# Optimization experiments

Measured on AMD Instinct MI355X. Metric: run time of the kernel, lower is better.

The kernel has to match this reference:

```python
import jax, jax.numpy as jnp
import numpy as np

B, S, E, D, H, L, V = 8, 128, 512, 1024, 16, 4, 32000
DH = D // H
FF = 4 * D
SCALE = 1.0 / (DH ** 0.5)
NEG = -1e30


def _layer_norm(x, g, b, eps=1e-5):
    m = jnp.mean(x, axis=-1, keepdims=True)
    v = jnp.mean((x - m) ** 2, axis=-1, keepdims=True)
    return (x - m) / jnp.sqrt(v + eps) * g + b


def _rel_shift(x):
    # x: [q, k, b, n] -> TransformerXL relative shift
    q, k, b, n = x.shape
    xp = jnp.concatenate([jnp.zeros((q, 1, b, n), x.dtype), x], axis=1)
    xp = xp.reshape(k + 1, q, b, n)
    return xp[1:].reshape(q, k, b, n)


def setup_inputs():
    key = jax.random.key(0)
    ks = jax.random.split(key, 40)
    g = lambda i, shape, s=0.02: jax.random.normal(ks[i], shape, jnp.float32) * s
    inp = {
        'input_ids': jax.random.randint(ks[0], (B, E), 0, V),
        'encoder_rep': jax.random.normal(ks[1], (B, E, D), jnp.float32),
        'input_mask': jnp.ones((B, E), jnp.float32),
        'decode_input': jax.random.randint(ks[2], (B, S), 0, V),
        'decode_target': jax.random.randint(ks[3], (B, S), 0, V),
        'word_emb': g(4, (V, D)),
        'qkv_w': g(5, (L, 3 * D, D)), 'r_w': g(6, (L, D, D)), 'o_w': g(7, (L, D, D)),
        'kv_w': g(8, (L, 2 * D, D)), 'q_w': g(9, (L, D, D)), 'io_w': g(10, (L, D, D)),
        'rr_bias': g(11, (L, H, DH)), 'rw_bias': g(12, (L, H, DH)),
        'ln1_g': jnp.ones((L, D)), 'ln1_b': jnp.zeros((L, D)),
        'ln2_g': jnp.ones((L, D)), 'ln2_b': jnp.zeros((L, D)),
        'ffn_w1': g(13, (L, FF, D)), 'ffn_b1': jnp.zeros((L, FF)),
        'ffn_w2': g(14, (L, D, FF)), 'ffn_b2': jnp.zeros((L, D)),
        'ln3_g': jnp.ones((L, D)), 'ln3_b': jnp.zeros((L, D)),
        'out_w': g(15, (D, D)), 'out_b': jnp.zeros((D,)),
        'copy_w': g(16, (D, D)), 'copy_b': jnp.zeros((D,)),
        'mode_w': g(17, (1, D)), 'mode_b': jnp.zeros((1,)),
    }
    return inp


def _forward(input_ids, encoder_rep, input_mask, decode_input, decode_target,
             word_emb, qkv_w, r_w, o_w, kv_w, q_w, io_w, rr_bias, rw_bias,
             ln1_g, ln1_b, ln2_g, ln2_b, ffn_w1, ffn_b1, ffn_w2, ffn_b2,
             ln3_g, ln3_b, out_w, out_b, copy_w, copy_b, mode_w, mode_b):
    # relative position embedding r: [S, D]
    pos_seq = jnp.arange(S - 1, -1, -1.0, dtype=jnp.float32)
    inv_freq = 1.0 / (10000.0 ** (jnp.arange(0.0, D, 2.0) / D))
    sin_inp = pos_seq[:, None] * inv_freq[None, :]
    r = jnp.concatenate([jnp.sin(sin_inp), jnp.cos(sin_inp)], axis=-1)

    causal = jnp.tril(jnp.ones((S, S), jnp.bool_))[:, :, None, None]  # [i,j,1,1]
    enc_mask_t = input_mask.T  # [E, B]

    core = word_emb[decode_input].transpose(1, 0, 2)  # [S, B, D]
    enc_t = encoder_rep.transpose(1, 0, 2)            # [E, B, D]

    for l in range(L):
        w = core
        heads = w @ qkv_w[l].T  # [S,B,3D]
        q, k, v = jnp.split(heads, 3, axis=-1)
        q = q.reshape(S, B, H, DH); k = k.reshape(S, B, H, DH); v = v.reshape(S, B, H, DH)
        r_k = (r @ r_w[l].T).reshape(S, H, DH)
        AC = jnp.einsum('ibnd,jbnd->ijbn', q + rw_bias[l], k)
        BD = _rel_shift(jnp.einsum('ibnd,jnd->ijbn', q + rr_bias[l], r_k))
        score = (AC + BD) * SCALE
        score = jnp.where(causal, score, NEG)
        prob = jax.nn.softmax(score, axis=1)
        vec = jnp.einsum('ijbn,jbnd->ibnd', prob, v).reshape(S, B, D)
        x = _layer_norm(w + vec @ o_w[l].T, ln1_g[l], ln1_b[l])

        # cross attention
        kv = enc_t @ kv_w[l].T
        k2, v2 = jnp.split(kv, 2, axis=-1)
        k2 = k2.reshape(E, B, H, DH); v2 = v2.reshape(E, B, H, DH)
        q2 = (x @ q_w[l].T).reshape(S, B, H, DH)
        score2 = jnp.einsum('qbnd,kbnd->qkbn', q2, k2) * SCALE
        score2 = score2 + (1.0 - enc_mask_t)[None, :, :, None] * NEG
        prob2 = jax.nn.softmax(score2, axis=1)
        vec2 = jnp.einsum('ijbn,jbnd->ibnd', prob2, v2).reshape(S, B, D)
        y = _layer_norm(x + vec2 @ io_w[l].T, ln2_g[l], ln2_b[l])

        # FFN (exact GELU as torch nn.GELU default)
        h = jax.nn.gelu(y @ ffn_w1[l].T + ffn_b1[l], approximate=False)
        h = h @ ffn_w2[l].T + ffn_b2[l]
        core = _layer_norm(y + h, ln3_g[l], ln3_b[l])

    core_out = core.transpose(1, 0, 2)  # [B, S, D]
    output = core_out @ out_w.T + out_b
    vocab_logits = output @ word_emb.T  # [B,S,V]
    vocab_prob = jax.nn.softmax(vocab_logits, axis=-1)

    copy_h = core_out @ copy_w.T + copy_b
    input_logits = jnp.einsum('bid,bjd->bij', copy_h, encoder_rep)
    input_logits = input_logits + (1.0 - input_mask[:, None, :]) * NEG
    input_prob = jax.nn.softmax(input_logits, axis=-1)  # [B,S,E]

    mode_sig = jax.nn.sigmoid(core_out @ mode_w.T + mode_b)  # [B,S,1]
    vocab_prob = vocab_prob * mode_sig

    idx = jnp.broadcast_to(input_ids[:, None, :], (B, S, E))
    b_i = jnp.arange(B)[:, None, None]
    s_i = jnp.arange(S)[None, :, None]
    vocab_prob = vocab_prob.at[b_i, s_i, idx].add((1.0 - mode_sig) * input_prob)

    flat = vocab_prob.reshape(-1, V)
    tgt = decode_target.reshape(-1)
    predict = jnp.take_along_axis(flat, tgt[:, None], axis=1)[:, 0]
    valid = (tgt != 0).astype(jnp.float32)
    loss = jnp.sum(-jnp.log(predict + 1e-6) * valid) / jnp.sum(valid)
    return jnp.repeat(loss[None], B)


def reference(input_ids, encoder_rep, input_mask, decode_input, decode_target,
              word_emb, qkv_w, r_w, o_w, kv_w, q_w, io_w, rr_bias, rw_bias,
              ln1_g, ln1_b, ln2_g, ln2_b, ffn_w1, ffn_b1, ffn_w2, ffn_b2,
              ln3_g, ln3_b, out_w, out_b, copy_w, copy_b, mode_w, mode_b):
    return _forward(input_ids, encoder_rep, input_mask, decode_input, decode_target,
                    word_emb, qkv_w, r_w, o_w, kv_w, q_w, io_w, rr_bias, rw_bias,
                    ln1_g, ln1_b, ln2_g, ln2_b, ffn_w1, ffn_b1, ffn_w2, ffn_b2,
                    ln3_g, ln3_b, out_w, out_b, copy_w, copy_b, mode_w, mode_b)
```

## Files before the change

kernel.cpp:

```cpp
#include <hip/hip_runtime.h>
#include <math.h>

#define B_ 8
#define S_ 128
#define E_ 512
#define D_ 1024
#define H_ 16
#define L_ 4
#define V_ 32000
#define DH_ 64
#define FF_ 4096
#define M_ 1024
#define ME_ 4096
#define NT_ 125
#define SCALE_F 0.125f
#define NEGV (-1e30f)

typedef __attribute__((ext_vector_type(8))) short short8;
typedef __attribute__((ext_vector_type(4))) float f32x4;

__device__ __forceinline__ float bf2f(ushort u) {
  union { unsigned int u32; float f; } v; v.u32 = ((unsigned int)u) << 16; return v.f;
}
__device__ __forceinline__ ushort f2bf(float x) {
  union { float f; unsigned int u; } v; v.f = x;
  unsigned int r = v.u + 0x7fff + ((v.u >> 16) & 1);
  return (ushort)(r >> 16);
}
__device__ __forceinline__ void gl_lds16(const ushort* g, ushort* l) {
  __builtin_amdgcn_global_load_lds((const __attribute__((address_space(1))) void*)g,
                                   (__attribute__((address_space(3))) void*)l, 16, 0, 0);
}

__device__ __forceinline__ float warp_reduce_sum(float v) {
#pragma unroll
  for (int o = 32; o > 0; o >>= 1) v += __shfl_down(v, o);
  return v;
}
__device__ __forceinline__ float warp_reduce_max(float v) {
#pragma unroll
  for (int o = 32; o > 0; o >>= 1) v = fmaxf(v, __shfl_down(v, o));
  return v;
}
__device__ __forceinline__ float block_reduce_sum(float v, float* sred) {
  v = warp_reduce_sum(v);
  __syncthreads();
  if ((threadIdx.x & 63) == 0) sred[threadIdx.x >> 6] = v;
  __syncthreads();
  float s = 0.0f;
  int nw = blockDim.x >> 6;
  for (int w = 0; w < nw; ++w) s += sred[w];
  return s;
}
__device__ __forceinline__ float block_reduce_max(float v, float* sred) {
  v = warp_reduce_max(v);
  __syncthreads();
  if ((threadIdx.x & 63) == 0) sred[threadIdx.x >> 6] = v;
  __syncthreads();
  float s = -3.4e38f;
  int nw = blockDim.x >> 6;
  for (int w = 0; w < nw; ++w) s = fmaxf(s, sred[w]);
  return s;
}

__global__ __launch_bounds__(256) void castf_kernel(const float* __restrict__ in,
                                                    ushort* __restrict__ out, int n4) {
  int t = blockIdx.x * 256 + threadIdx.x;
  if (t >= n4) return;
  float4 v = ((const float4*)in)[t];
  ushort4 o;
  o.x = f2bf(v.x); o.y = f2bf(v.y); o.z = f2bf(v.z); o.w = f2bf(v.w);
  ((ushort4*)out)[t] = o;
}

__global__ __launch_bounds__(256) void castlayer_kernel(
    const float* __restrict__ sqkv, const float* __restrict__ so,
    const float* __restrict__ sq, const float* __restrict__ sio,
    const float* __restrict__ sf1, const float* __restrict__ sf2,
    ushort* __restrict__ dqkv, ushort* __restrict__ dov,
    ushort* __restrict__ dq, ushort* __restrict__ dio,
    ushort* __restrict__ df1, ushort* __restrict__ df2) {
  int t = blockIdx.x * 256 + threadIdx.x;
  const float* src; ushort* dst; int idx;
  if (t < 786432)       { src = sqkv; dst = dqkv; idx = t; }
  else if (t < 1048576) { src = so;  dst = dov; idx = t - 786432; }
  else if (t < 1310720) { src = sq;  dst = dq;  idx = t - 1048576; }
  else if (t < 1572864) { src = sio; dst = dio; idx = t - 1310720; }
  else if (t < 2621440) { src = sf1; dst = df1; idx = t - 1572864; }
  else if (t < 3670016) { src = sf2; dst = df2; idx = t - 2621440; }
  else return;
  float4 v = ((const float4*)src)[idx];
  ushort4 o4;
  o4.x = f2bf(v.x); o4.y = f2bf(v.y); o4.z = f2bf(v.z); o4.w = f2bf(v.w);
  ((ushort4*)dst)[idx] = o4;
}

__global__ __launch_bounds__(256) void enct_kernel(const float* __restrict__ enc,
                                                   ushort* __restrict__ encT) {
  int t = blockIdx.x * 256 + threadIdx.x;
  if (t >= ME_ * D_) return;
  int d = t & (D_ - 1);
  int row = t >> 10;
  int e = row >> 3, b = row & 7;
  encT[t] = f2bf(enc[((size_t)b * E_ + e) * D_ + d]);
}

__global__ __launch_bounds__(256) void pos_emb_kernel(ushort* __restrict__ r) {
  int t = blockIdx.x * 256 + threadIdx.x;
  if (t >= S_ * D_) return;
  int i = t / D_, j = t % D_;
  float pos = (float)(S_ - 1 - i);
  int jj = (j < D_ / 2) ? j : (j - D_ / 2);
  float invf = powf(10000.0f, -(float)(2 * jj) / (float)D_);
  float a = pos * invf;
  r[t] = f2bf((j < D_ / 2) ? sinf(a) : cosf(a));
}

__global__ __launch_bounds__(256) void embed_kernel(const int* __restrict__ ids,
                                                    const float* __restrict__ emb,
                                                    float* __restrict__ core,
                                                    ushort* __restrict__ core_bf) {
  int t = blockIdx.x * 256 + threadIdx.x;
  if (t >= M_ * D_) return;
  int d = t & (D_ - 1);
  int row = t >> 10;
  int s = row >> 3, b = row & 7;
  float v = emb[(size_t)ids[b * S_ + s] * D_ + d];
  core[t] = v;
  core_bf[t] = f2bf(v);
}

template <int EPI>
__global__ __launch_bounds__(256) void gemm_w_kernel(
    const ushort* __restrict__ A, const ushort* __restrict__ Bm,
    const float* __restrict__ bias, void* __restrict__ Cv,
    int M, int N, int K, int ksplit,
    long long Arow, long long Abatch, long long Brow, long long Bbatch,
    long long Crow, long long Cbatch, long long Csplit) {
  __shared__ ushort lA[128 * 32];
  __shared__ ushort lB[128 * 32];
  int tid = threadIdx.x;
  int bz = blockIdx.z;
  int batch = bz / ksplit, split = bz % ksplit;
  int kLen = K / ksplit, kStart = split * kLen;
  const ushort* Ab = A + (size_t)batch * Abatch;
  const ushort* Bb = Bm + (size_t)batch * Bbatch;
  int bm = blockIdx.y * 128, bn = blockIdx.x * 128;
  int lane = tid & 63, wave = tid >> 6;
  int wrow = (wave >> 1) * 64, wcol = (wave & 1) * 64;
  int quad = lane >> 4, l16 = lane & 15;
  f32x4 acc[4][4];
#pragma unroll
  for (int i = 0; i < 4; ++i)
#pragma unroll
    for (int j = 0; j < 4; ++j) { acc[i][j][0] = 0.f; acc[i][j][1] = 0.f; acc[i][j][2] = 0.f; acc[i][j][3] = 0.f; }
  int r0 = tid >> 2, c0 = (tid & 3) * 8;
  int r1 = (tid + 256) >> 2;
  for (int k0 = kStart; k0 < kStart + kLen; k0 += 32) {
    __syncthreads();
    gl_lds16(Ab + (size_t)(bm + r0) * Arow + k0 + c0, &lA[(size_t)tid * 8]);
    gl_lds16(Ab + (size_t)(bm + r1) * Arow + k0 + c0, &lA[(size_t)(256 + tid) * 8]);
    gl_lds16(Bb + (size_t)(bn + r0) * Brow + k0 + c0, &lB[(size_t)tid * 8]);
    gl_lds16(Bb + (size_t)(bn + r1) * Brow + k0 + c0, &lB[(size_t)(256 + tid) * 8]);
    __syncthreads();
    short8 af[4], bfr[4];
#pragma unroll
    for (int mi = 0; mi < 4; ++mi)
      af[mi] = *(const short8*)&lA[(size_t)(wrow + mi * 16 + l16) * 32 + quad * 8];
#pragma unroll
    for (int ni = 0; ni < 4; ++ni)
      bfr[ni] = *(const short8*)&lB[(size_t)(wcol + ni * 16 + l16) * 32 + quad * 8];
#pragma unroll
    for (int mi = 0; mi < 4; ++mi)
#pragma unroll
      for (int ni = 0; ni < 4; ++ni)
        acc[mi][ni] = __builtin_amdgcn_mfma_f32_16x16x32_bf16(af[mi], bfr[ni], acc[mi][ni], 0, 0, 0);
  }
#pragma unroll
  for (int mi = 0; mi < 4; ++mi) {
    int row0 = bm + wrow + mi * 16 + quad * 4;
#pragma unroll
    for (int ni = 0; ni < 4; ++ni) {
      int col = bn + wcol + ni * 16 + l16;
      float bv = 0.f;
      if (EPI >= 3) bv = bias[col];
#pragma unroll
      for (int r = 0; r < 4; ++r) {
        float v = acc[mi][ni][r] + bv;
        if (EPI == 4) v = 0.5f * v * (1.0f + erff(v * 0.70710678118654752f));
        size_t ci = (size_t)split * Csplit + (size_t)batch * Cbatch + (size_t)(row0 + r) * Crow + col;
        if (EPI == 0) ((float*)Cv)[ci] = v;
        else ((ushort*)Cv)[ci] = f2bf(v);
      }
    }
  }
}

template <int EPI>
__global__ __launch_bounds__(512, 2) void gemm256_kernel(
    const ushort* __restrict__ A, const ushort* __restrict__ Bm, void* __restrict__ Cv,
    float* __restrict__ tmax, float* __restrict__ tsum,
    long long Arow, long long Abatch, long long Brow, long long Bbatch,
    long long Crow, long long Cbatch) {
  __shared__ ushort sT[4][2][2][128 * 32];
  __shared__ float smax[256][4];
  __shared__ float ssum[256][4];
  const int NK = 32;
  int tid = threadIdx.x;
  int bm, bn, bnT = 0, batch = 0;
  if constexpr (EPI == 5) {
    int orig = blockIdx.x;
    int xcd = orig & 7;
    int base = (xcd < 4) ? xcd * 63 : 4 * 63 + (xcd - 4) * 62;
    int wg = base + (orig >> 3);
    bm = (wg & 3) * 256;
    bnT = wg >> 2;
    bn = bnT * 256;
  } else {
    bn = blockIdx.x * 256;
    bm = blockIdx.y * 256;
    batch = blockIdx.z;
  }
  const ushort* Ab = A + (size_t)batch * Abatch;
  const ushort* Bb = Bm + (size_t)batch * Bbatch;
  int lane = tid & 63, wave = tid >> 6;
  int wr = wave >> 2;
  int wc = wave & 3;
  int bhalf = wc >> 1;
  int brow0 = (wc & 1) * 64;
  int quad = lane >> 4, l16 = lane & 15;
  int sr = tid >> 2, sc = (tid & 3) * 8;

  f32x4 acc[8][4];
#pragma unroll
  for (int i = 0; i < 8; ++i)
#pragma unroll
    for (int j = 0; j < 4; ++j) { acc[i][j][0]=0.f; acc[i][j][1]=0.f; acc[i][j][2]=0.f; acc[i][j][3]=0.f; }

#define STAGE_HALF(s_, ab_, h_)                                                        \
  do {                                                                                 \
    int s__ = (s_); int b__ = s__ & 3;                                                 \
    if ((ab_) == 0)                                                                    \
      gl_lds16(Ab + (size_t)(bm + (h_) * 128 + sr) * Arow + s__ * 32 + sc,             \
               &sT[b__][0][h_][tid * 8]);                                              \
    else                                                                               \
      gl_lds16(Bb + (size_t)(bn + (h_) * 128 + sr) * Brow + s__ * 32 + sc,             \
               &sT[b__][1][h_][tid * 8]);                                              \
  } while (0)

#pragma unroll
  for (int s = 0; s < 3; ++s) {
    STAGE_HALF(s, 0, 0); STAGE_HALF(s, 0, 1);
    STAGE_HALF(s, 1, 0); STAGE_HALF(s, 1, 1);
  }
  asm volatile("s_waitcnt vmcnt(8)");
  __builtin_amdgcn_s_barrier();
  __builtin_amdgcn_sched_barrier(0);

  short8 af[4], bfv[4];
  for (int t = 0; t < NK; ++t) {
    int bt = t & 3;
#pragma unroll
    for (int i = 0; i < 4; ++i)
      af[i] = *(const short8*)&sT[bt][0][wr][(i * 16 + l16) * 32 + quad * 8];
#pragma unroll
    for (int i = 0; i < 4; ++i)
      bfv[i] = *(const short8*)&sT[bt][1][bhalf][(brow0 + i * 16 + l16) * 32 + quad * 8];
    if (t + 3 < NK) { STAGE_HALF(t + 3, 0, 0); STAGE_HALF(t + 3, 0, 1); }
    __builtin_amdgcn_s_barrier();
    __builtin_amdgcn_sched_barrier(0);
    __builtin_amdgcn_s_setprio(1);
#pragma unroll
    for (int mi = 0; mi < 4; ++mi)
#pragma unroll
      for (int ni = 0; ni < 4; ++ni)
        acc[mi][ni] = __builtin_amdgcn_mfma_f32_16x16x32_bf16(af[mi], bfv[ni], acc[mi][ni], 0, 0, 0);
    __builtin_amdgcn_s_setprio(0);
    __builtin_amdgcn_s_barrier();
    __builtin_amdgcn_sched_barrier(0);
#pragma unroll
    for (int i = 0; i < 4; ++i)
      af[i] = *(const short8*)&sT[bt][0][wr][((4 + i) * 16 + l16) * 32 + quad * 8];
    if (t + 3 < NK) { STAGE_HALF(t + 3, 1, 0); STAGE_HALF(t + 3, 1, 1); }
    if (t + 3 < NK)      asm volatile("s_waitcnt vmcnt(8)");
    else if (t + 2 < NK) asm volatile("s_waitcnt vmcnt(4)");
    else                 asm volatile("s_waitcnt vmcnt(0)");
    __builtin_amdgcn_s_barrier();
    __builtin_amdgcn_sched_barrier(0);
    __builtin_amdgcn_s_setprio(1);
#pragma unroll
    for (int mi = 0; mi < 4; ++mi)
#pragma unroll
      for (int ni = 0; ni < 4; ++ni)
        acc[4 + mi][ni] = __builtin_amdgcn_mfma_f32_16x16x32_bf16(af[mi], bfv[ni], acc[4 + mi][ni], 0, 0, 0);
    __builtin_amdgcn_s_setprio(0);
    __builtin_amdgcn_s_barrier();
    __builtin_amdgcn_sched_barrier(0);
  }
#undef STAGE_HALF

  if constexpr (EPI == 5) {
#pragma unroll
    for (int mi = 0; mi < 8; ++mi)
#pragma unroll
      for (int r = 0; r < 4; ++r) {
        int rr = wr * 128 + mi * 16 + quad * 4 + r;
        float lm = -3.4e38f;
#pragma unroll
        for (int ni = 0; ni < 4; ++ni) lm = fmaxf(lm, acc[mi][ni][r]);
#pragma unroll
        for (int o = 1; o < 16; o <<= 1) lm = fmaxf(lm, __shfl_xor(lm, o));
        if (l16 == 0) smax[rr][wc] = lm;
      }
    __syncthreads();
#pragma unroll
    for (int mi = 0; mi < 8; ++mi)
#pragma unroll
      for (int r = 0; r < 4; ++r) {
        int rr = wr * 128 + mi * 16 + quad * 4 + r;
        float m = fmaxf(fmaxf(smax[rr][0], smax[rr][1]), fmaxf(smax[rr][2], smax[rr][3]));
        float ls = 0.f;
#pragma unroll
        for (int ni = 0; ni < 4; ++ni) ls += __expf(acc[mi][ni][r] - m);
#pragma unroll
        for (int o = 1; o < 16; o <<= 1) ls += __shfl_xor(ls, o);
        if (l16 == 0) ssum[rr][wc] = ls;
      }
    __syncthreads();
    if (tid < 256) {
      float m = fmaxf(fmaxf(smax[tid][0], smax[tid][1]), fmaxf(smax[tid][2], smax[tid][3]));
      float s = ssum[tid][0] + ssum[tid][1] + ssum[tid][2] + ssum[tid][3];
      tmax[(size_t)(bm + tid) * NT_ + bnT] = m;
      tsum[(size_t)(bm + tid) * NT_ + bnT] = s;
    }
  } else {
    ushort* C = (ushort*)Cv + (size_t)batch * Cbatch;
#pragma unroll
    for (int mi = 0; mi < 8; ++mi) {
      int row0 = bm + wr * 128 + mi * 16 + quad * 4;
#pragma unroll
      for (int ni = 0; ni < 4; ++ni) {
        int col = bn + wc * 64 + ni * 16 + l16;
#pragma unroll
        for (int r = 0; r < 4; ++r)
          C[(size_t)(row0 + r) * Crow + col] = f2bf(acc[mi][ni][r]);
      }
    }
  }
}

__global__ __launch_bounds__(256) void vocab_combine_kernel(const float* __restrict__ tmax,
                                                            const float* __restrict__ tsum,
                                                            float* __restrict__ rmax,
                                                            float* __restrict__ rsum) {
  __shared__ float sred[4];
  int m = blockIdx.x;
  float mx = -3.4e38f;
  for (int t = threadIdx.x; t < NT_; t += 256) mx = fmaxf(mx, tmax[(size_t)m * NT_ + t]);
  mx = block_reduce_max(mx, sred);
  float s = 0.f;
  for (int t = threadIdx.x; t < NT_; t += 256)
    s += tsum[(size_t)m * NT_ + t] * expf(tmax[(size_t)m * NT_ + t] - mx);
  s = block_reduce_sum(s, sred);
  if (threadIdx.x == 0) { rmax[m] = mx; rsum[m] = s; }
}

__global__ __launch_bounds__(256) void tlogit_kernel(const ushort* __restrict__ headout,
                                                     const ushort* __restrict__ emb,
                                                     const int* __restrict__ tgt,
                                                     float* __restrict__ tl) {
  __shared__ float sred[4];
  int m = blockIdx.x;
  int s = m >> 3, b = m & 7;
  int t = tgt[b * S_ + s];
  const ushort* a = headout + (size_t)m * 2048;
  const ushort* w = emb + (size_t)t * D_;
  float acc = 0.f;
  for (int i = threadIdx.x; i < D_; i += 256) acc += bf2f(a[i]) * bf2f(w[i]);
  acc = block_reduce_sum(acc, sred);
  if (threadIdx.x == 0) tl[m] = acc;
}

__global__ __launch_bounds__(256) void attn1_fused_kernel(const ushort* __restrict__ heads,
                                                          const ushort* __restrict__ rkproj,
                                                          const float* __restrict__ rw,
                                                          const float* __restrict__ rr,
                                                          ushort* __restrict__ attnA) {
  __shared__ float score[128][129];
  __shared__ ushort pP[128][136];
  __shared__ ushort vT[64][136];
  int bz = blockIdx.x;
  int b = bz >> 4, n = bz & 15;
  int tid = threadIdx.x, lane = tid & 63, wave = tid >> 6;
  int quad = lane >> 4, l16 = lane & 15;
  int wrow = wave * 32;

  {
    int j = tid >> 1, dbase = (tid & 1) * 32;
    const ushort* src = heads + (size_t)(j * 8 + b) * 3072 + 2048 + n * 64 + dbase;
#pragma unroll
    for (int c8 = 0; c8 < 4; ++c8) {
      short8 v8 = *(const short8*)(src + c8 * 8);
#pragma unroll
      for (int cc = 0; cc < 8; ++cc) vT[dbase + c8 * 8 + cc][j] = (ushort)v8[cc];
    }
  }

  short8 qrw[2][2], qrr[2][2];
#pragma unroll
  for (int mi = 0; mi < 2; ++mi) {
    int i = wrow + mi * 16 + l16;
    const ushort* qp = heads + (size_t)(i * 8 + b) * 3072 + n * 64;
#pragma unroll
    for (int kc = 0; kc < 2; ++kc) {
      int k0 = kc * 32 + quad * 8;
      short8 qv = *(const short8*)(qp + k0);
      short8 w, rv;
#pragma unroll
      for (int t = 0; t < 8; ++t) {
        float q = bf2f((ushort)qv[t]);
        w[t] = (short)f2bf(q + rw[n * 64 + k0 + t]);
        rv[t] = (short)f2bf(q + rr[n * 64 + k0 + t]);
      }
      qrw[mi][kc] = w; qrr[mi][kc] = rv;
    }
  }

  {
    f32x4 acc[2][8];
#pragma unroll
    for (int i = 0; i < 2; ++i)
#pragma unroll
      for (int j = 0; j < 8; ++j) { acc[i][j][0]=0.f; acc[i][j][1]=0.f; acc[i][j][2]=0.f; acc[i][j][3]=0.f; }
#pragma unroll
    for (int kc = 0; kc < 2; ++kc) {
      int k0 = kc * 32 + quad * 8;
      short8 kf[8];
#pragma unroll
      for (int ni = 0; ni < 8; ++ni) {
        int j = ni * 16 + l16;
        kf[ni] = *(const short8*)(heads + (size_t)(j * 8 + b) * 3072 + 1024 + n * 64 + k0);
      }
#pragma unroll
      for (int mi = 0; mi < 2; ++mi)
#pragma unroll
        for (int ni = 0; ni < 8; ++ni)
          acc[mi][ni] = __builtin_amdgcn_mfma_f32_16x16x32_bf16(qrw[mi][kc], kf[ni], acc[mi][ni], 0, 0, 0);
    }
#pragma unroll
    for (int mi = 0; mi < 2; ++mi)
#pragma unroll
      for (int ni = 0; ni < 8; ++ni)
#pragma unroll
        for (int r = 0; r < 4; ++r)
          score[wrow + mi * 16 + quad * 4 + r][ni * 16 + l16] = acc[mi][ni][r];
  }
  {
    f32x4 acc[2][8];
#pragma unroll
    for (int i = 0; i < 2; ++i)
#pragma unroll
      for (int j = 0; j < 8; ++j) { acc[i][j][0]=0.f; acc[i][j][1]=0.f; acc[i][j][2]=0.f; acc[i][j][3]=0.f; }
#pragma unroll
    for (int kc = 0; kc < 2; ++kc) {
      int k0 = kc * 32 + quad * 8;
      short8 rkf[8];
#pragma unroll
      for (int ni = 0; ni < 8; ++ni) {
        int jp = ni * 16 + l16;
        rkf[ni] = *(const short8*)(rkproj + (size_t)jp * 1024 + n * 64 + k0);
      }
#pragma unroll
      for (int mi = 0; mi < 2; ++mi)
#pragma unroll
        for (int ni = 0; ni < 8; ++ni)
          acc[mi][ni] = __builtin_amdgcn_mfma_f32_16x16x32_bf16(qrr[mi][kc], rkf[ni], acc[mi][ni], 0, 0, 0);
    }
#pragma unroll
    for (int mi = 0; mi < 2; ++mi)
#pragma unroll
      for (int r = 0; r < 4; ++r) {
        int i = wrow + mi * 16 + quad * 4 + r;
#pragma unroll
        for (int ni = 0; ni < 8; ++ni) {
          int jp = ni * 16 + l16;
          if (jp >= 127 - i) score[i][jp - 127 + i] += acc[mi][ni][r];
        }
      }
  }
  {
    int row = tid >> 1, halfc = (tid & 1) * 64;
    float mx = -3.4e38f;
    for (int c = halfc; c < halfc + 64; ++c) {
      float v = (c <= row) ? score[row][c] * SCALE_F : -3.4e38f;
      mx = fmaxf(mx, v);
    }
    mx = fmaxf(mx, __shfl_xor(mx, 1));
    float s = 0.f;
    for (int c = halfc; c < halfc + 64; ++c) {
      float e = (c <= row) ? __expf(score[row][c] * SCALE_F - mx) : 0.f;
      score[row][c] = e;
      s += e;
    }
    s += __shfl_xor(s, 1);
    float inv = 1.0f / s;
    for (int c = halfc; c < halfc + 64; ++c) pP[row][c] = f2bf(score[row][c] * inv);
  }
  __syncthreads();
  {
    f32x4 acc[2][4];
#pragma unroll
    for (int i = 0; i < 2; ++i)
#pragma unroll
      for (int j = 0; j < 4; ++j) { acc[i][j][0]=0.f; acc[i][j][1]=0.f; acc[i][j][2]=0.f; acc[i][j][3]=0.f; }
#pragma unroll
    for (int kc = 0; kc < 4; ++kc) {
      int k0 = kc * 32 + quad * 8;
      short8 pf[2], vf[4];
#pragma unroll
      for (int mi = 0; mi < 2; ++mi)
        pf[mi] = *(const short8*)&pP[wrow + mi * 16 + l16][k0];
#pragma unroll
      for (int ni = 0; ni < 4; ++ni)
        vf[ni] = *(const short8*)&vT[ni * 16 + l16][k0];
#pragma unroll
      for (int mi = 0; mi < 2; ++mi)
#pragma unroll
        for (int ni = 0; ni < 4; ++ni)
          acc[mi][ni] = __builtin_amdgcn_mfma_f32_16x16x32_bf16(pf[mi], vf[ni], acc[mi][ni], 0, 0, 0);
    }
#pragma unroll
    for (int mi = 0; mi < 2; ++mi)
#pragma unroll
      for (int r = 0; r < 4; ++r) {
        int i = wrow + mi * 16 + quad * 4 + r;
#pragma unroll
        for (int ni = 0; ni < 4; ++ni)
          attnA[(size_t)(i * 8 + b) * 1024 + n * 64 + ni * 16 + l16] = f2bf(acc[mi][ni][r]);
      }
  }
}

__global__ __launch_bounds__(256) void attn2_fused_kernel(const float* __restrict__ q0,
                                                          const float* __restrict__ q1,
                                                          const ushort* __restrict__ kvproj,
                                                          const float* __restrict__ mask,
                                                          ushort* __restrict__ attnA) {
  __shared__ ushort vT[64][136];
  __shared__ ushort pP[128][136];
  __shared__ float mtile[128];
  int bz = blockIdx.x;
  int b = bz >> 4, n = bz & 15;
  int tid = threadIdx.x, lane = tid & 63, wave = tid >> 6;
  int quad = lane >> 4, l16 = lane & 15;
  int wrow = wave * 32;
  short8 qf[2][2];
#pragma unroll
  for (int mi = 0; mi < 2; ++mi) {
    int i = wrow + mi * 16 + l16;
    size_t base = (size_t)(i * 8 + b) * 1024 + n * 64;
#pragma unroll
    for (int kc = 0; kc < 2; ++kc) {
      int k0 = kc * 32 + quad * 8;
      short8 v;
#pragma unroll
      for (int t = 0; t < 8; ++t) v[t] = (short)f2bf(q0[base + k0 + t] + q1[base + k0 + t]);
      qf[mi][kc] = v;
    }
  }
  float m_run[2][4], l_run[2][4];
#pragma unroll
  for (int mi = 0; mi < 2; ++mi)
#pragma unroll
    for (int r = 0; r < 4; ++r) { m_run[mi][r] = -3.0e38f; l_run[mi][r] = 0.f; }
  f32x4 accO[2][4];
#pragma unroll
  for (int i = 0; i < 2; ++i)
#pragma unroll
    for (int j = 0; j < 4; ++j) { accO[i][j][0]=0.f; accO[i][j][1]=0.f; accO[i][j][2]=0.f; accO[i][j][3]=0.f; }

  for (int et = 0; et < 4; ++et) {
    __syncthreads();
    {
      int j = tid >> 1, dbase = (tid & 1) * 32;
      int e = et * 128 + j;
      const ushort* src = kvproj + (size_t)(e * 8 + b) * 2048 + 1024 + n * 64 + dbase;
#pragma unroll
      for (int c8 = 0; c8 < 4; ++c8) {
        short8 v8 = *(const short8*)(src + c8 * 8);
#pragma unroll
        for (int cc = 0; cc < 8; ++cc) vT[dbase + c8 * 8 + cc][j] = (ushort)v8[cc];
      }
      if (tid < 128) mtile[tid] = (1.0f - mask[b * E_ + et * 128 + tid]) * NEGV;
    }
    f32x4 accS[2][8];
#pragma unroll
    for (int i = 0; i < 2; ++i)
#pragma unroll
      for (int j = 0; j < 8; ++j) { accS[i][j][0]=0.f; accS[i][j][1]=0.f; accS[i][j][2]=0.f; accS[i][j][3]=0.f; }
#pragma unroll
    for (int kc = 0; kc < 2; ++kc) {
      int k0 = kc * 32 + quad * 8;
      short8 kf[8];
#pragma unroll
      for (int ni = 0; ni < 8; ++ni) {
        int e = et * 128 + ni * 16 + l16;
        kf[ni] = *(const short8*)(kvproj + (size_t)(e * 8 + b) * 2048 + n * 64 + k0);
      }
#pragma unroll
      for (int mi = 0; mi < 2; ++mi)
#pragma unroll
        for (int ni = 0; ni < 8; ++ni)
          accS[mi][ni] = __builtin_amdgcn_mfma_f32_16x16x32_bf16(qf[mi][kc], kf[ni], accS[mi][ni], 0, 0, 0);
    }
    __syncthreads();
#pragma unroll
    for (int mi = 0; mi < 2; ++mi)
#pragma unroll
      for (int r = 0; r < 4; ++r) {
        float v[8];
        float vmax = -3.4e38f;
#pragma unroll
        for (int ni = 0; ni < 8; ++ni) {
          v[ni] = accS[mi][ni][r] * SCALE_F + mtile[ni * 16 + l16];
          vmax = fmaxf(vmax, v[ni]);
        }
#pragma unroll
        for (int o = 1; o < 16; o <<= 1) vmax = fmaxf(vmax, __shfl_xor(vmax, o));
        float mnew = fmaxf(m_run[mi][r], vmax);
        float alpha = __expf(m_run[mi][r] - mnew);
        float ls = 0.f;
        int row = wrow + mi * 16 + quad * 4 + r;
#pragma unroll
        for (int ni = 0; ni < 8; ++ni) {
          float p = __expf(v[ni] - mnew);
          ls += p;
          pP[row][ni * 16 + l16] = f2bf(p);
        }
#pragma unroll
        for (int o = 1; o < 16; o <<= 1) ls += __shfl_xor(ls, o);
        l_run[mi][r] = l_run[mi][r] * alpha + ls;
        m_run[mi][r] = mnew;
#pragma unroll
        for (int ni = 0; ni < 4; ++ni) accO[mi][ni][r] *= alpha;
      }
#pragma unroll
    for (int kc = 0; kc < 4; ++kc) {
      int k0 = kc * 32 + quad * 8;
      short8 pf[2], vf[4];
#pragma unroll
      for (int mi = 0; mi < 2; ++mi)
        pf[mi] = *(const short8*)&pP[wrow + mi * 16 + l16][k0];
#pragma unroll
      for (int ni = 0; ni < 4; ++ni)
        vf[ni] = *(const short8*)&vT[ni * 16 + l16][k0];
#pragma unroll
      for (int mi = 0; mi < 2; ++mi)
#pragma unroll
        for (int ni = 0; ni < 4; ++ni)
          accO[mi][ni] = __builtin_amdgcn_mfma_f32_16x16x32_bf16(pf[mi], vf[ni], accO[mi][ni], 0, 0, 0);
    }
  }
#pragma unroll
  for (int mi = 0; mi < 2; ++mi)
#pragma unroll
    for (int r = 0; r < 4; ++r) {
      int i = wrow + mi * 16 + quad * 4 + r;
      float inv = 1.0f / l_run[mi][r];
#pragma unroll
      for (int ni = 0; ni < 4; ++ni)
        attnA[(size_t)(i * 8 + b) * 1024 + n * 64 + ni * 16 + l16] = f2bf(accO[mi][ni][r] * inv);
    }
}

__global__ __launch_bounds__(256) void addln_kernel(const float* __restrict__ a,
                                                    const float* __restrict__ c,
                                                    int nsplit, long long cstride,
                                                    const float* __restrict__ bias,
                                                    const float* __restrict__ g,
                                                    const float* __restrict__ bb,
                                                    float* __restrict__ out,
                                                    ushort* __restrict__ out_bf) {
  __shared__ float sred[4];
  int row = blockIdx.x;
  const float* pa = a + (size_t)row * D_;
  float vals[4];
  float s = 0.f;
#pragma unroll
  for (int it = 0; it < 4; ++it) {
    int idx = threadIdx.x + it * 256;
    float v = pa[idx];
    for (int sp = 0; sp < nsplit; ++sp) v += c[(size_t)sp * cstride + (size_t)row * D_ + idx];
    if (bias) v += bias[idx];
    vals[it] = v;
    s += v;
  }
  s = block_reduce_sum(s, sred);
  float mean = s * (1.0f / D_);
  float ss = 0.f;
#pragma unroll
  for (int it = 0; it < 4; ++it) {
    float dd = vals[it] - mean;
    ss += dd * dd;
  }
  ss = block_reduce_sum(ss, sred);
  float inv = rsqrtf(ss * (1.0f / D_) + 1e-5f);
#pragma unroll
  for (int it = 0; it < 4; ++it) {
    int idx = threadIdx.x + it * 256;
    float r = (vals[it] - mean) * inv * g[idx] + bb[idx];
    out[(size_t)row * D_ + idx] = r;
    out_bf[(size_t)row * D_ + idx] = f2bf(r);
  }
}

__global__ __launch_bounds__(256) void mode_kernel(const float* __restrict__ core,
                                                   const float* __restrict__ mode_w,
                                                   const float* __restrict__ mode_b,
                                                   float* __restrict__ mode_sig) {
  __shared__ float sred[4];
  int m = blockIdx.x;
  const float* a = core + (size_t)m * D_;
  float s = 0.f;
  for (int t = threadIdx.x; t < D_; t += 256) s += a[t] * mode_w[t];
  s = block_reduce_sum(s, sred);
  if (threadIdx.x == 0) mode_sig[m] = 1.0f / (1.0f + expf(-(s + mode_b[0])));
}

__global__ __launch_bounds__(256) void final_kernel(const float* __restrict__ lg,
                                                    const int* __restrict__ ids,
                                                    const float* __restrict__ mask,
                                                    const int* __restrict__ tgt,
                                                    const float* __restrict__ mode_sig,
                                                    const float* __restrict__ tlogit,
                                                    const float* __restrict__ rmax,
                                                    const float* __restrict__ rsum,
                                                    float* __restrict__ loss_acc) {
  __shared__ float sred[4];
  int s = blockIdx.x, b = blockIdx.y;
  int m = s * B_ + b;
  size_t base = (size_t)(b * S_ + s) * E_;
  const long long LGS = (long long)B_ * S_ * E_;
  int tg = tgt[b * S_ + s];
  float lv[2];
  float mx = -3.4e38f;
#pragma unroll
  for (int it = 0; it < 2; ++it) {
    int e = threadIdx.x + it * 256;
    float raw = 0.f;
#pragma unroll
    for (int sp = 0; sp < 4; ++sp) raw += lg[sp * LGS + base + e];
    raw += (1.0f - mask[b * E_ + e]) * NEGV;
    lv[it] = raw;
    mx = fmaxf(mx, raw);
  }
  mx = block_reduce_max(mx, sred);
  float ssum = 0.f, csum = 0.f;
#pragma unroll
  for (int it = 0; it < 2; ++it) {
    int e = threadIdx.x + it * 256;
    float ev = expf(lv[it] - mx);
    ssum += ev;
    if (ids[b * E_ + e] == tg) csum += ev;
  }
  ssum = block_reduce_sum(ssum, sred);
  csum = block_reduce_sum(csum, sred);
  if (threadIdx.x == 0) {
    float copy_p = csum / ssum;
    float pv = expf(tlogit[m] - rmax[m]) / rsum[m];
    float msig = mode_sig[m];
    float predict = pv * msig + (1.0f - msig) * copy_p;
    float valid = (tg != 0) ? 1.0f : 0.0f;
    atomicAdd(&loss_acc[0], -logf(predict + 1e-6f) * valid);
    atomicAdd(&loss_acc[1], valid);
  }
}

__global__ void writeout_kernel(const float* __restrict__ loss_acc, float* __restrict__ out) {
  if (threadIdx.x < B_) out[threadIdx.x] = loss_acc[0] / loss_acc[1];
}

static void gw(hipStream_t st, int epi, const ushort* A, const ushort* B, const float* bias,
               void* C, int M, int N, int K,
               long long Ar, long long Ab, long long Br, long long Bb,
               long long Cr, long long Cb, int nb, int ksplit, long long Csplit) {
  dim3 g(N / 128, M / 128, nb * ksplit);
  switch (epi) {
    case 0: gemm_w_kernel<0><<<g, 256, 0, st>>>(A, B, bias, C, M, N, K, ksplit, Ar, Ab, Br, Bb, Cr, Cb, Csplit); break;
    case 1: gemm_w_kernel<1><<<g, 256, 0, st>>>(A, B, bias, C, M, N, K, ksplit, Ar, Ab, Br, Bb, Cr, Cb, Csplit); break;
    case 3: gemm_w_kernel<3><<<g, 256, 0, st>>>(A, B, bias, C, M, N, K, ksplit, Ar, Ab, Br, Bb, Cr, Cb, Csplit); break;
    case 4: gemm_w_kernel<4><<<g, 256, 0, st>>>(A, B, bias, C, M, N, K, ksplit, Ar, Ab, Br, Bb, Cr, Cb, Csplit); break;
  }
}
static void castTo(hipStream_t st, const float* src, ushort* dst, size_t count) {
  int n4 = (int)(count / 4);
  castf_kernel<<<(n4 + 255) / 256, 256, 0, st>>>(src, dst, n4);
}

extern "C" void kernel_launch(void* const* d_in, const int* in_sizes, int n_in,
                              void* d_out, int out_size, void* d_ws, size_t ws_size,
                              hipStream_t stream) {
  const int* input_ids = (const int*)d_in[0];
  const float* encoder_rep = (const float*)d_in[1];
  const float* input_mask = (const float*)d_in[2];
  const int* decode_input = (const int*)d_in[3];
  const int* decode_target = (const int*)d_in[4];
  const float* word_emb = (const float*)d_in[5];
  const float* qkv_w = (const float*)d_in[6];
  const float* r_w = (const float*)d_in[7];
  const float* o_w = (const float*)d_in[8];
  const float* kv_w = (const float*)d_in[9];
  const float* q_w = (const float*)d_in[10];
  const float* io_w = (const float*)d_in[11];
  const float* rr_bias = (const float*)d_in[12];
  const float* rw_bias = (const float*)d_in[13];
  const float* ln1_g = (const float*)d_in[14];
  const float* ln1_b = (const float*)d_in[15];
  const float* ln2_g = (const float*)d_in[16];
  const float* ln2_b = (const float*)d_in[17];
  const float* ffn_w1 = (const float*)d_in[18];
  const float* ffn_b1 = (const float*)d_in[19];
  const float* ffn_w2 = (const float*)d_in[20];
  const float* ffn_b2 = (const float*)d_in[21];
  const float* ln3_g = (const float*)d_in[22];
  const float* ln3_b = (const float*)d_in[23];
  const float* out_w = (const float*)d_in[24];
  const float* out_b = (const float*)d_in[25];
  const float* copy_w = (const float*)d_in[26];
  const float* copy_b = (const float*)d_in[27];
  const float* mode_w = (const float*)d_in[28];
  const float* mode_b = (const float*)d_in[29];
  float* out = (float*)d_out;

  char* base = (char*)d_ws;
  size_t off = 0;
  auto alloc = [&](size_t bytes) -> void* {
    void* p = base + off;
    off = (off + bytes + 255) & ~(size_t)255;
    return p;
  };

  ushort* wl_qkv = (ushort*)alloc((size_t)3 * D_ * D_ * 2);
  ushort* wl_o = (ushort*)alloc((size_t)D_ * D_ * 2);
  ushort* wl_q = (ushort*)alloc((size_t)D_ * D_ * 2);
  ushort* wl_io = (ushort*)alloc((size_t)D_ * D_ * 2);
  ushort* wl_f1 = (ushort*)alloc((size_t)FF_ * D_ * 2);
  ushort* wl_f2 = (ushort*)alloc((size_t)FF_ * D_ * 2);
  ushort* wl_kv = (ushort*)alloc((size_t)L_ * 2 * D_ * D_ * 2);
  ushort* wl_r = (ushort*)alloc((size_t)L_ * D_ * D_ * 2);
  ushort* kvproj_bf = (ushort*)alloc((size_t)L_ * ME_ * 2 * D_ * 2);
  ushort* rkproj_bf = (ushort*)alloc((size_t)L_ * S_ * D_ * 2);

  ushort* w_emb = (ushort*)alloc((size_t)V_ * D_ * 2);
  ushort* w_oc = (ushort*)alloc((size_t)2048 * D_ * 2);
  float* b_oc = (float*)alloc(2048 * 4);
  ushort* enc_bf = (ushort*)alloc((size_t)ME_ * D_ * 2);
  ushort* encT_bf = (ushort*)alloc((size_t)ME_ * D_ * 2);
  ushort* r_bf = (ushort*)alloc((size_t)S_ * D_ * 2);
  float* f_core = (float*)alloc((size_t)M_ * D_ * 4);
  ushort* core_bf = (ushort*)alloc((size_t)M_ * D_ * 2);
  ushort* heads_bf = (ushort*)alloc((size_t)M_ * 3 * D_ * 2);
  ushort* attnA_bf = (ushort*)alloc((size_t)M_ * D_ * 2);
  float* f_tmp = (float*)alloc((size_t)4 * M_ * D_ * 4);
  float* f_x = (float*)alloc((size_t)M_ * D_ * 4);
  ushort* x_bf = (ushort*)alloc((size_t)M_ * D_ * 2);
  float* f_y = (float*)alloc((size_t)M_ * D_ * 4);
  ushort* y_bf = (ushort*)alloc((size_t)M_ * D_ * 2);
  float* f_q = (float*)alloc((size_t)2 * M_ * D_ * 4);
  ushort* ffnh_bf = (ushort*)alloc((size_t)M_ * FF_ * 2);
  ushort* headout_bf = (ushort*)alloc((size_t)M_ * 2048 * 2);
  float* f_lg = (float*)alloc((size_t)4 * B_ * S_ * E_ * 4);
  float* f_tmax = (float*)alloc((size_t)M_ * NT_ * 4);
  float* f_tsum = (float*)alloc((size_t)M_ * NT_ * 4);
  float* f_rmax = (float*)alloc(M_ * 4);
  float* f_rsum = (float*)alloc(M_ * 4);
  float* f_tlogit = (float*)alloc(M_ * 4);
  float* f_mode = (float*)alloc(M_ * 4);
  float* f_loss = (float*)alloc(64);

  castTo(stream, word_emb, w_emb, (size_t)V_ * D_);
  castTo(stream, out_w, w_oc, (size_t)D_ * D_);
  castTo(stream, copy_w, w_oc + (size_t)D_ * D_, (size_t)D_ * D_);
  hipMemcpyAsync(b_oc, out_b, D_ * 4, hipMemcpyDeviceToDevice, stream);
  hipMemcpyAsync(b_oc + D_, copy_b, D_ * 4, hipMemcpyDeviceToDevice, stream);
  castTo(stream, encoder_rep, enc_bf, (size_t)ME_ * D_);
  enct_kernel<<<(ME_ * D_) / 256, 256, 0, stream>>>(encoder_rep, encT_bf);
  pos_emb_kernel<<<(S_ * D_ + 255) / 256, 256, 0, stream>>>(r_bf);
  embed_kernel<<<(M_ * D_) / 256, 256, 0, stream>>>(decode_input, word_emb, f_core, core_bf);

  castTo(stream, kv_w, wl_kv, (size_t)L_ * 2 * D_ * D_);
  castTo(stream, r_w, wl_r, (size_t)L_ * D_ * D_);
  gemm256_kernel<1><<<dim3(2 * D_ / 256, ME_ / 256, L_), 512, 0, stream>>>(
      encT_bf, wl_kv, kvproj_bf, nullptr, nullptr,
      D_, 0, D_, (long long)2 * D_ * D_, 2 * D_, (long long)ME_ * 2 * D_);
  gw(stream, 1, r_bf, wl_r, nullptr, rkproj_bf, S_, D_, D_,
     D_, 0, D_, (long long)D_ * D_, D_, (long long)S_ * D_, L_, 1, 0);

  for (int l = 0; l < L_; ++l) {
    castlayer_kernel<<<14336, 256, 0, stream>>>(
        qkv_w + (size_t)l * 3 * D_ * D_, o_w + (size_t)l * D_ * D_,
        q_w + (size_t)l * D_ * D_, io_w + (size_t)l * D_ * D_,
        ffn_w1 + (size_t)l * FF_ * D_, ffn_w2 + (size_t)l * FF_ * D_,
        wl_qkv, wl_o, wl_q, wl_io, wl_f1, wl_f2);

    gw(stream, 1, core_bf, wl_qkv, nullptr, heads_bf, M_, 3 * D_, D_, D_, 0, D_, 0, 3 * D_, 0, 1, 1, 0);
    attn1_fused_kernel<<<B_ * H_, 256, 0, stream>>>(heads_bf, rkproj_bf + (size_t)l * S_ * D_,
                                                    rw_bias + (size_t)l * D_,
                                                    rr_bias + (size_t)l * D_, attnA_bf);
    gw(stream, 0, attnA_bf, wl_o, nullptr, f_tmp, M_, D_, D_, D_, 0, D_, 0, D_, 0, 1, 2,
       (long long)M_ * D_);
    addln_kernel<<<M_, 256, 0, stream>>>(f_core, f_tmp, 2, (long long)M_ * D_, nullptr,
                                         ln1_g + (size_t)l * D_, ln1_b + (size_t)l * D_, f_x, x_bf);

    gw(stream, 0, x_bf, wl_q, nullptr, f_q, M_, D_, D_, D_, 0, D_, 0, D_, 0, 1, 2,
       (long long)M_ * D_);
    attn2_fused_kernel<<<B_ * H_, 256, 0, stream>>>(f_q, f_q + (size_t)M_ * D_,
                                                    kvproj_bf + (size_t)l * ME_ * 2 * D_,
                                                    input_mask, attnA_bf);
    gw(stream, 0, attnA_bf, wl_io, nullptr, f_tmp, M_, D_, D_, D_, 0, D_, 0, D_, 0, 1, 2,
       (long long)M_ * D_);
    addln_kernel<<<M_, 256, 0, stream>>>(f_x, f_tmp, 2, (long long)M_ * D_, nullptr,
                                         ln2_g + (size_t)l * D_, ln2_b + (size_t)l * D_, f_y, y_bf);

    gw(stream, 4, y_bf, wl_f1, ffn_b1 + (size_t)l * FF_, ffnh_bf, M_, FF_, D_, D_, 0, D_, 0, FF_, 0, 1, 1, 0);
    gw(stream, 0, ffnh_bf, wl_f2, nullptr, f_tmp, M_, D_, FF_, FF_, 0, FF_, 0, D_, 0, 1, 4,
       (long long)M_ * D_);
    addln_kernel<<<M_, 256, 0, stream>>>(f_y, f_tmp, 4, (long long)M_ * D_,
                                         ffn_b2 + (size_t)l * D_,
                                         ln3_g + (size_t)l * D_, ln3_b + (size_t)l * D_, f_core, core_bf);
  }

  gw(stream, 3, core_bf, w_oc, b_oc, headout_bf, M_, 2048, D_, D_, 0, D_, 0, 2048, 0, 1, 1, 0);
  mode_kernel<<<M_, 256, 0, stream>>>(f_core, mode_w, mode_b, f_mode);

  gemm256_kernel<5><<<500, 512, 0, stream>>>(headout_bf, w_emb, nullptr, f_tmax, f_tsum,
                                             2048, 0, D_, 0, 0, 0);
  vocab_combine_kernel<<<M_, 256, 0, stream>>>(f_tmax, f_tsum, f_rmax, f_rsum);
  tlogit_kernel<<<M_, 256, 0, stream>>>(headout_bf, w_emb, decode_target, f_tlogit);

  gw(stream, 0, headout_bf + D_, enc_bf, nullptr, f_lg, S_, E_, D_,
     (long long)B_ * 2048, 2048, D_, (long long)E_ * D_, E_, (long long)S_ * E_, B_, 4,
     (long long)B_ * S_ * E_);

  hipMemsetAsync(f_loss, 0, 2 * sizeof(float), stream);
  final_kernel<<<dim3(S_, B_), 256, 0, stream>>>(f_lg, input_ids, input_mask, decode_target,
                                                 f_mode, f_tlogit, f_rmax, f_rsum, f_loss);
  writeout_kernel<<<1, 64, 0, stream>>>(f_loss, out);
}
```

Measured before the change: 1.588 ms.

## Swizzle GEMM LDS layout and fuse small encoder, mode, and tlogit kernels

```diff
diff --git a/kernel.cpp b/kernel.cpp
--- a/kernel.cpp
+++ b/kernel.cpp
@@ -95,14 +95,17 @@
   ((ushort4*)dst)[idx] = o4;
 }
 
-__global__ __launch_bounds__(256) void enct_kernel(const float* __restrict__ enc,
-                                                   ushort* __restrict__ encT) {
+__global__ __launch_bounds__(256) void enc_both_kernel(const float* __restrict__ enc,
+                                                       ushort* __restrict__ enc_bf,
+                                                       ushort* __restrict__ encT) {
   int t = blockIdx.x * 256 + threadIdx.x;
   if (t >= ME_ * D_) return;
+  ushort bv = f2bf(enc[t]);
+  enc_bf[t] = bv;
   int d = t & (D_ - 1);
-  int row = t >> 10;
-  int e = row >> 3, b = row & 7;
-  encT[t] = f2bf(enc[((size_t)b * E_ + e) * D_ + d]);
+  int be = t >> 10;
+  int b = be >> 9, e = be & (E_ - 1);
+  encT[((size_t)(e * B_ + b) << 10) + d] = bv;
 }
 
 __global__ __launch_bounds__(256) void pos_emb_kernel(ushort* __restrict__ r) {
@@ -229,7 +232,9 @@
   int bhalf = wc >> 1;
   int brow0 = (wc & 1) * 64;
   int quad = lane >> 4, l16 = lane & 15;
-  int sr = tid >> 2, sc = (tid & 3) * 8;
+  int sr = tid >> 2;
+  int sslot = (((tid & 3) ^ ((sr >> 1) & 3)) * 8);
+  int rsw = (quad ^ ((l16 >> 1) & 3)) * 8;
 
   f32x4 acc[8][4];
 #pragma unroll
@@ -241,10 +246,10 @@
   do {                                                                                 \
     int s__ = (s_); int b__ = s__ & 3;                                                 \
     if ((ab_) == 0)                                                                    \
-      gl_lds16(Ab + (size_t)(bm + (h_) * 128 + sr) * Arow + s__ * 32 + sc,             \
+      gl_lds16(Ab + (size_t)(bm + (h_) * 128 + sr) * Arow + s__ * 32 + sslot,          \
                &sT[b__][0][h_][tid * 8]);                                              \
     else                                                                               \
-      gl_lds16(Bb + (size_t)(bn + (h_) * 128 + sr) * Brow + s__ * 32 + sc,             \
+      gl_lds16(Bb + (size_t)(bn + (h_) * 128 + sr) * Brow + s__ * 32 + sslot,          \
                &sT[b__][1][h_][tid * 8]);                                              \
   } while (0)
 
@@ -262,10 +267,10 @@
     int bt = t & 3;
 #pragma unroll
     for (int i = 0; i < 4; ++i)
-      af[i] = *(const short8*)&sT[bt][0][wr][(i * 16 + l16) * 32 + quad * 8];
+      af[i] = *(const short8*)&sT[bt][0][wr][(i * 16 + l16) * 32 + rsw];
 #pragma unroll
     for (int i = 0; i < 4; ++i)
-      bfv[i] = *(const short8*)&sT[bt][1][bhalf][(brow0 + i * 16 + l16) * 32 + quad * 8];
+      bfv[i] = *(const short8*)&sT[bt][1][bhalf][(brow0 + i * 16 + l16) * 32 + rsw];
     if (t + 3 < NK) { STAGE_HALF(t + 3, 0, 0); STAGE_HALF(t + 3, 0, 1); }
     __builtin_amdgcn_s_barrier();
     __builtin_amdgcn_sched_barrier(0);
@@ -280,7 +285,7 @@
     __builtin_amdgcn_sched_barrier(0);
 #pragma unroll
     for (int i = 0; i < 4; ++i)
-      af[i] = *(const short8*)&sT[bt][0][wr][((4 + i) * 16 + l16) * 32 + quad * 8];
+      af[i] = *(const short8*)&sT[bt][0][wr][((4 + i) * 16 + l16) * 32 + rsw];
     if (t + 3 < NK) { STAGE_HALF(t + 3, 1, 0); STAGE_HALF(t + 3, 1, 1); }
     if (t + 3 < NK)      asm volatile("s_waitcnt vmcnt(8)");
     else if (t + 2 < NK) asm volatile("s_waitcnt vmcnt(4)");
@@ -351,8 +356,12 @@
 
 __global__ __launch_bounds__(256) void vocab_combine_kernel(const float* __restrict__ tmax,
                                                             const float* __restrict__ tsum,
+                                                            const ushort* __restrict__ headout,
+                                                            const ushort* __restrict__ emb,
+                                                            const int* __restrict__ tgt,
                                                             float* __restrict__ rmax,
-                                                            float* __restrict__ rsum) {
+                                                            float* __restrict__ rsum,
+                                                            float* __restrict__ tl) {
   __shared__ float sred[4];
   int m = blockIdx.x;
   float mx = -3.4e38f;
@@ -362,23 +371,14 @@
   for (int t = threadIdx.x; t < NT_; t += 256)
     s += tsum[(size_t)m * NT_ + t] * expf(tmax[(size_t)m * NT_ + t] - mx);
   s = block_reduce_sum(s, sred);
-  if (threadIdx.x == 0) { rmax[m] = mx; rsum[m] = s; }
-}
-
-__global__ __launch_bounds__(256) void tlogit_kernel(const ushort* __restrict__ headout,
-                                                     const ushort* __restrict__ emb,
-                                                     const int* __restrict__ tgt,
-                                                     float* __restrict__ tl) {
-  __shared__ float sred[4];
-  int m = blockIdx.x;
-  int s = m >> 3, b = m & 7;
-  int t = tgt[b * S_ + s];
+  int si = m >> 3, b = m & 7;
+  int t = tgt[b * S_ + si];
   const ushort* a = headout + (size_t)m * 2048;
   const ushort* w = emb + (size_t)t * D_;
   float acc = 0.f;
   for (int i = threadIdx.x; i < D_; i += 256) acc += bf2f(a[i]) * bf2f(w[i]);
   acc = block_reduce_sum(acc, sred);
-  if (threadIdx.x == 0) tl[m] = acc;
+  if (threadIdx.x == 0) { rmax[m] = mx; rsum[m] = s; tl[m] = acc; }
 }
 
 __global__ __launch_bounds__(256) void attn1_fused_kernel(const ushort* __restrict__ heads,
@@ -680,7 +680,10 @@
                                                     const float* __restrict__ g,
                                                     const float* __restrict__ bb,
                                                     float* __restrict__ out,
-                                                    ushort* __restrict__ out_bf) {
+                                                    ushort* __restrict__ out_bf,
+                                                    const float* __restrict__ mw,
+                                                    const float* __restrict__ mb,
+                                                    float* __restrict__ msig) {
   __shared__ float sred[4];
   int row = blockIdx.x;
   const float* pa = a + (size_t)row * D_;
@@ -709,22 +712,20 @@
   for (int it = 0; it < 4; ++it) {
     int idx = threadIdx.x + it * 256;
     float r = (vals[it] - mean) * inv * g[idx] + bb[idx];
+    vals[it] = r;
     out[(size_t)row * D_ + idx] = r;
     out_bf[(size_t)row * D_ + idx] = f2bf(r);
   }
-}
-
-__global__ __launch_bounds__(256) void mode_kernel(const float* __restrict__ core,
-                                                   const float* __restrict__ mode_w,
-                                                   const float* __restrict__ mode_b,
-                                                   float* __restrict__ mode_sig) {
-  __shared__ float sred[4];
-  int m = blockIdx.x;
-  const float* a = core + (size_t)m * D_;
-  float s = 0.f;
-  for (int t = threadIdx.x; t < D_; t += 256) s += a[t] * mode_w[t];
-  s = block_reduce_sum(s, sred);
-  if (threadIdx.x == 0) mode_sig[m] = 1.0f / (1.0f + expf(-(s + mode_b[0])));
+  if (mw) {
+    float sm = 0.f;
+#pragma unroll
+    for (int it = 0; it < 4; ++it) {
+      int idx = threadIdx.x + it * 256;
+      sm += vals[it] * mw[idx];
+    }
+    sm = block_reduce_sum(sm, sred);
+    if (threadIdx.x == 0) msig[row] = 1.0f / (1.0f + expf(-(sm + mb[0])));
+  }
 }
 
 __global__ __launch_bounds__(256) void final_kernel(const float* __restrict__ lg,
@@ -883,8 +884,7 @@
   castTo(stream, copy_w, w_oc + (size_t)D_ * D_, (size_t)D_ * D_);
   hipMemcpyAsync(b_oc, out_b, D_ * 4, hipMemcpyDeviceToDevice, stream);
   hipMemcpyAsync(b_oc + D_, copy_b, D_ * 4, hipMemcpyDeviceToDevice, stream);
-  castTo(stream, encoder_rep, enc_bf, (size_t)ME_ * D_);
-  enct_kernel<<<(ME_ * D_) / 256, 256, 0, stream>>>(encoder_rep, encT_bf);
+  enc_both_kernel<<<(ME_ * D_) / 256, 256, 0, stream>>>(encoder_rep, enc_bf, encT_bf);
   pos_emb_kernel<<<(S_ * D_ + 255) / 256, 256, 0, stream>>>(r_bf);
   embed_kernel<<<(M_ * D_) / 256, 256, 0, stream>>>(decode_input, word_emb, f_core, core_bf);
 
@@ -910,7 +910,8 @@
     gw(stream, 0, attnA_bf, wl_o, nullptr, f_tmp, M_, D_, D_, D_, 0, D_, 0, D_, 0, 1, 2,
        (long long)M_ * D_);
     addln_kernel<<<M_, 256, 0, stream>>>(f_core, f_tmp, 2, (long long)M_ * D_, nullptr,
-                                         ln1_g + (size_t)l * D_, ln1_b + (size_t)l * D_, f_x, x_bf);
+                                         ln1_g + (size_t)l * D_, ln1_b + (size_t)l * D_, f_x, x_bf,
+                                         nullptr, nullptr, nullptr);
 
     gw(stream, 0, x_bf, wl_q, nullptr, f_q, M_, D_, D_, D_, 0, D_, 0, D_, 0, 1, 2,
        (long long)M_ * D_);
@@ -920,23 +921,26 @@
     gw(stream, 0, attnA_bf, wl_io, nullptr, f_tmp, M_, D_, D_, D_, 0, D_, 0, D_, 0, 1, 2,
        (long long)M_ * D_);
     addln_kernel<<<M_, 256, 0, stream>>>(f_x, f_tmp, 2, (long long)M_ * D_, nullptr,
-                                         ln2_g + (size_t)l * D_, ln2_b + (size_t)l * D_, f_y, y_bf);
+                                         ln2_g + (size_t)l * D_, ln2_b + (size_t)l * D_, f_y, y_bf,
+                                         nullptr, nullptr, nullptr);
 
     gw(stream, 4, y_bf, wl_f1, ffn_b1 + (size_t)l * FF_, ffnh_bf, M_, FF_, D_, D_, 0, D_, 0, FF_, 0, 1, 1, 0);
     gw(stream, 0, ffnh_bf, wl_f2, nullptr, f_tmp, M_, D_, FF_, FF_, 0, FF_, 0, D_, 0, 1, 4,
        (long long)M_ * D_);
+    bool last = (l == L_ - 1);
     addln_kernel<<<M_, 256, 0, stream>>>(f_y, f_tmp, 4, (long long)M_ * D_,
                                          ffn_b2 + (size_t)l * D_,
-                                         ln3_g + (size_t)l * D_, ln3_b + (size_t)l * D_, f_core, core_bf);
+                                         ln3_g + (size_t)l * D_, ln3_b + (size_t)l * D_, f_core, core_bf,
+                                         last ? mode_w : nullptr, last ? mode_b : nullptr,
+                                         last ? f_mode : nullptr);
   }
 
   gw(stream, 3, core_bf, w_oc, b_oc, headout_bf, M_, 2048, D_, D_, 0, D_, 0, 2048, 0, 1, 1, 0);
-  mode_kernel<<<M_, 256, 0, stream>>>(f_core, mode_w, mode_b, f_mode);
 
   gemm256_kernel<5><<<500, 512, 0, stream>>>(headout_bf, w_emb, nullptr, f_tmax, f_tsum,
                                              2048, 0, D_, 0, 0, 0);
-  vocab_combine_kernel<<<M_, 256, 0, stream>>>(f_tmax, f_tsum, f_rmax, f_rsum);
-  tlogit_kernel<<<M_, 256, 0, stream>>>(headout_bf, w_emb, decode_target, f_tlogit);
+  vocab_combine_kernel<<<M_, 256, 0, stream>>>(f_tmax, f_tsum, headout_bf, w_emb, decode_target,
+                                               f_rmax, f_rsum, f_tlogit);
 
   gw(stream, 0, headout_bf + D_, enc_bf, nullptr, f_lg, S_, E_, D_,
      (long long)B_ * 2048, 2048, D_, (long long)E_ * D_, E_, (long long)S_ * E_, B_, 4,
```

Result: no change. 1.573 ms (-0.9%).
